# Optimization experiments

Measured on AMD Instinct MI355X. Metric: run time of the kernel, lower is better.

## Reference

```python
import jax, jax.numpy as jnp
import numpy as np

BATCH, IN_F, OUT_F = 8192, 4096, 4096


def setup_inputs() -> dict:
    key = jax.random.key(0)
    kx, kw = jax.random.split(key)
    x = jax.random.normal(kx, (BATCH, IN_F), dtype=jnp.float32)
    # weights binarized to {-1, +1} as in __init__ (uniform(-1,1) then sign)
    W = jnp.where(jax.random.normal(kw, (OUT_F, IN_F)) > 0, 1.0, -1.0).astype(jnp.float32)
    return {"x": x, "W": W}


def reference(x, W):
    # forward: input thresholded to {0,1} (x>0 -> 1, else 0), then x_bin @ W^T, no bias
    x_bin = (x > 0).astype(x.dtype)
    return jnp.matmul(x_bin, W.T)  # [batch, out_features]
```

## Files before the change

### kernel.cpp

```cpp
#include <hip/hip_runtime.h>
#include <stdint.h>

typedef __attribute__((ext_vector_type(4)))  int   v4i;
typedef __attribute__((ext_vector_type(8)))  int   v8i;
typedef __attribute__((ext_vector_type(16))) float v16f;

#define BATCH 8192
#define KDIM  4096
#define NOUT  4096
#define KB    (KDIM / 2)
#define BK_B  128
#define NT    (KDIM / 256)

__global__ __launch_bounds__(256) void pack_x4(const float* __restrict__ x,
                                               uint32_t* __restrict__ xb) {
    int t = blockIdx.x * 256 + threadIdx.x;
    const float4* p = (const float4*)x + (size_t)t * 2;
    float4 f0 = p[0];
    float4 f1 = p[1];
    uint32_t b = (f0.x > 0.f ? 0x2u        : 0u)
               | (f0.y > 0.f ? 0x20u       : 0u)
               | (f0.z > 0.f ? 0x200u      : 0u)
               | (f0.w > 0.f ? 0x2000u     : 0u)
               | (f1.x > 0.f ? 0x20000u    : 0u)
               | (f1.y > 0.f ? 0x200000u   : 0u)
               | (f1.z > 0.f ? 0x2000000u  : 0u)
               | (f1.w > 0.f ? 0x20000000u : 0u);
    xb[t] = b;
}

__global__ __launch_bounds__(256) void pack_w4(const float* __restrict__ w,
                                               uint32_t* __restrict__ wb) {
    int t = blockIdx.x * 256 + threadIdx.x;
    const float4* p = (const float4*)w + (size_t)t * 2;
    float4 f0 = p[0];
    float4 f1 = p[1];
    uint32_t b = (f0.x > 0.f ? 0x2u        : 0xAu)
               | (f0.y > 0.f ? 0x20u       : 0xA0u)
               | (f0.z > 0.f ? 0x200u      : 0xA00u)
               | (f0.w > 0.f ? 0x2000u     : 0xA000u)
               | (f1.x > 0.f ? 0x20000u    : 0xA0000u)
               | (f1.y > 0.f ? 0x200000u   : 0xA00000u)
               | (f1.z > 0.f ? 0x2000000u  : 0xA000000u)
               | (f1.w > 0.f ? 0x20000000u : 0xA0000000u);
    wb[t] = b;
}

__global__ __launch_bounds__(256, 2) void bin_gemm4(const uint8_t* __restrict__ A,
                                                    const uint8_t* __restrict__ B,
                                                    float* __restrict__ C) {
    __shared__ __align__(16) uint8_t sm[49152];

    const int tid  = threadIdx.x;
    const int w    = tid >> 6;
    const int lane = tid & 63;
    const int l31  = lane & 31;
    const int kc   = lane >> 5;
    const int rsw  = lane & 7;

    const int Mbase = blockIdx.y * 256;
    const int Nbase = blockIdx.x * 128;
    const int wm = (w >> 1) * 128;
    const int wn = (w & 1) * 64;

    const int grow = lane >> 3;
    const int swz  = ((lane & 7) ^ ((lane >> 3) & 7)) * 16;

    const uint8_t* pA = A + (size_t)(Mbase + w * 64 + grow) * KB + swz;
    const uint8_t* pB = B + (size_t)(Nbase + w * 32 + grow) * KB + swz;
    uint8_t* sA = sm;
    uint8_t* sB = sm + 32768;

    v16f acc[4][2] = {};

    for (int t = 0; t < NT; ++t) {
        const int kof = t * BK_B;

        #pragma unroll
        for (int L = 0; L < 8; ++L)
            __builtin_amdgcn_global_load_lds(
                (__attribute__((address_space(1))) void*)(pA + (size_t)(L * 8) * KB + kof),
                (__attribute__((address_space(3))) void*)(sA + (w * 64 + L * 8) * 128),
                16, 0, 0);
        #pragma unroll
        for (int L = 0; L < 4; ++L)
            __builtin_amdgcn_global_load_lds(
                (__attribute__((address_space(1))) void*)(pB + (size_t)(L * 8) * KB + kof),
                (__attribute__((address_space(3))) void*)(sB + (w * 32 + L * 8) * 128),
                16, 0, 0);
        __syncthreads();

        #pragma unroll
        for (int ks = 0; ks < 4; ++ks) {
            const int slot = ((ks * 2 + kc) ^ rsw) * 16;
            v4i bf[2];
            #pragma unroll
            for (int nb = 0; nb < 2; ++nb)
                bf[nb] = *(const v4i*)(sB + (wn + nb * 32 + l31) * 128 + slot);
            #pragma unroll
            for (int mb = 0; mb < 4; ++mb) {
                v4i af = *(const v4i*)(sA + (wm + mb * 32 + l31) * 128 + slot);
                v8i a8 = {af[0], af[1], af[2], af[3], 0, 0, 0, 0};
                #pragma unroll
                for (int nb = 0; nb < 2; ++nb) {
                    v8i b8 = {bf[nb][0], bf[nb][1], bf[nb][2], bf[nb][3], 0, 0, 0, 0};
                    acc[mb][nb] = __builtin_amdgcn_mfma_scale_f32_32x32x64_f8f6f4(
                        a8, b8, acc[mb][nb], 4, 4,
                        0, 0x7F7F7F7F, 0, 0x7F7F7F7F);
                }
            }
        }
        __syncthreads();
    }

    float* Cp = C + (size_t)(Mbase + wm + 4 * kc) * NOUT + (Nbase + wn + l31);
    #pragma unroll
    for (int mb = 0; mb < 4; ++mb)
        #pragma unroll
        for (int nb = 0; nb < 2; ++nb)
            #pragma unroll
            for (int r = 0; r < 16; ++r)
                Cp[(size_t)(mb * 32 + (r & 3) + 8 * (r >> 2)) * NOUT + nb * 32]
                    = acc[mb][nb][r];
}

extern "C" void kernel_launch(void* const* d_in, const int* in_sizes, int n_in,
                              void* d_out, int out_size, void* d_ws, size_t ws_size,
                              hipStream_t stream) {
    const float* x = (const float*)d_in[0];
    const float* W = (const float*)d_in[1];
    float* out = (float*)d_out;

    uint8_t* xb = (uint8_t*)d_ws;
    uint8_t* wb = (uint8_t*)d_ws + (size_t)BATCH * KDIM / 2;

    pack_x4<<<(BATCH * (size_t)KDIM / 8) / 256, 256, 0, stream>>>(x, (uint32_t*)xb);
    pack_w4<<<((size_t)NOUT * KDIM / 8) / 256, 256, 0, stream>>>(W, (uint32_t*)wb);

    dim3 grid(NOUT / 128, BATCH / 256);
    bin_gemm4<<<grid, 256, 0, stream>>>(xb, wb, out);
}
```

Measured before the change: 330.2 us.

## Pre-swizzle W into MFMA fragment layout, load B directly to registers, double-buffer A

The weight packing kernel now writes W in a fragment-major layout, so each lane can load its MFMA B operands straight from global memory into registers with one 16-byte read, with no LDS staging. The GEMM block grows to 512 threads over a 256x256 tile, and A tiles are double-buffered in LDS, with the next tile's async global-to-LDS load issued before computing on the current one. This aims to cut LDS traffic and sync stalls and to hide A load latency. In exchange it adds register pressure from the 8 per-iteration B fragment loads and relies on L2 for B reuse across blocks that share an N column.

```diff
diff --git a/kernel.cpp b/kernel.cpp
--- a/kernel.cpp
+++ b/kernel.cpp
@@ -29,27 +29,35 @@
     xb[t] = b;
 }
 
-__global__ __launch_bounds__(256) void pack_w4(const float* __restrict__ w,
-                                               uint32_t* __restrict__ wb) {
-    int t = blockIdx.x * 256 + threadIdx.x;
-    const float4* p = (const float4*)w + (size_t)t * 2;
-    float4 f0 = p[0];
-    float4 f1 = p[1];
-    uint32_t b = (f0.x > 0.f ? 0x2u        : 0xAu)
-               | (f0.y > 0.f ? 0x20u       : 0xA0u)
-               | (f0.z > 0.f ? 0x200u      : 0xA00u)
-               | (f0.w > 0.f ? 0x2000u     : 0xA000u)
-               | (f1.x > 0.f ? 0x20000u    : 0xA0000u)
-               | (f1.y > 0.f ? 0x200000u   : 0xA00000u)
-               | (f1.z > 0.f ? 0x2000000u  : 0xA000000u)
-               | (f1.w > 0.f ? 0x20000000u : 0xA0000000u);
-    wb[t] = b;
+__global__ __launch_bounds__(256) void pack_wf(const float* __restrict__ w,
+                                               uint32_t* __restrict__ wf) {
+    int u = blockIdx.x * 256 + threadIdx.x;
+    int lane = u & 63;
+    int T    = (u >> 6) & 63;
+    int g    = u >> 12;
+    const float* src = w + (size_t)(g * 32 + (lane & 31)) * KDIM
+                         + T * 64 + (lane >> 5) * 32;
+    uint32_t wd[4];
+    #pragma unroll
+    for (int i = 0; i < 4; ++i) {
+        float4 f0 = ((const float4*)src)[i * 2];
+        float4 f1 = ((const float4*)src)[i * 2 + 1];
+        wd[i] = (f0.x > 0.f ? 0x2u        : 0xAu)
+              | (f0.y > 0.f ? 0x20u       : 0xA0u)
+              | (f0.z > 0.f ? 0x200u      : 0xA00u)
+              | (f0.w > 0.f ? 0x2000u     : 0xA000u)
+              | (f1.x > 0.f ? 0x20000u    : 0xA0000u)
+              | (f1.y > 0.f ? 0x200000u   : 0xA00000u)
+              | (f1.z > 0.f ? 0x2000000u  : 0xA000000u)
+              | (f1.w > 0.f ? 0x20000000u : 0xA0000000u);
+    }
+    ((uint4*)wf)[u] = make_uint4(wd[0], wd[1], wd[2], wd[3]);
 }
 
-__global__ __launch_bounds__(256, 2) void bin_gemm4(const uint8_t* __restrict__ A,
-                                                    const uint8_t* __restrict__ B,
+__global__ __launch_bounds__(512, 2) void bin_gemm4(const uint8_t* __restrict__ A,
+                                                    const uint8_t* __restrict__ Bf,
                                                     float* __restrict__ C) {
-    __shared__ __align__(16) uint8_t sm[49152];
+    __shared__ __align__(16) uint8_t sm[65536];
 
     const int tid  = threadIdx.x;
     const int w    = tid >> 6;
@@ -59,57 +67,66 @@
     const int rsw  = lane & 7;
 
     const int Mbase = blockIdx.y * 256;
-    const int Nbase = blockIdx.x * 128;
-    const int wm = (w >> 1) * 128;
-    const int wn = (w & 1) * 64;
+    const int Nbase = blockIdx.x * 256;
+    const int wm = (w >> 2) * 128;
+    const int wn = (w & 3) * 64;
 
-    const int grow = lane >> 3;
+    const int srow = w * 32 + (lane >> 3);
     const int swz  = ((lane & 7) ^ ((lane >> 3) & 7)) * 16;
+    const uint8_t* pA = A + (size_t)(Mbase + srow) * KB + swz;
 
-    const uint8_t* pA = A + (size_t)(Mbase + w * 64 + grow) * KB + swz;
-    const uint8_t* pB = B + (size_t)(Nbase + w * 32 + grow) * KB + swz;
-    uint8_t* sA = sm;
-    uint8_t* sB = sm + 32768;
+    const uint8_t* pBf = Bf + (size_t)((Nbase + wn) >> 5) * 65536 + (size_t)lane * 16;
 
     v16f acc[4][2] = {};
 
+    #pragma unroll
+    for (int L = 0; L < 4; ++L)
+        __builtin_amdgcn_global_load_lds(
+            (__attribute__((address_space(1))) void*)(pA + (size_t)(L * 8) * KB),
+            (__attribute__((address_space(3))) void*)(sm + (w * 32 + L * 8) * 128),
+            16, 0, 0);
+    __syncthreads();
+
     for (int t = 0; t < NT; ++t) {
-        const int kof = t * BK_B;
+        v4i bfr[2][4];
+        #pragma unroll
+        for (int nb = 0; nb < 2; ++nb)
+            #pragma unroll
+            for (int ks = 0; ks < 4; ++ks)
+                bfr[nb][ks] = *(const v4i*)(pBf + (size_t)(nb * 64 + t * 4 + ks) * 1024);
 
-        #pragma unroll
-        for (int L = 0; L < 8; ++L)
-            __builtin_amdgcn_global_load_lds(
-                (__attribute__((address_space(1))) void*)(pA + (size_t)(L * 8) * KB + kof),
-                (__attribute__((address_space(3))) void*)(sA + (w * 64 + L * 8) * 128),
-                16, 0, 0);
-        #pragma unroll
-        for (int L = 0; L < 4; ++L)
-            __builtin_amdgcn_global_load_lds(
-                (__attribute__((address_space(1))) void*)(pB + (size_t)(L * 8) * KB + kof),
-                (__attribute__((address_space(3))) void*)(sB + (w * 32 + L * 8) * 128),
-                16, 0, 0);
-        __syncthreads();
+        if (t + 1 < NT) {
+            const int nbuf = (t + 1) & 1;
+            const int kof  = (t + 1) * BK_B;
+            #pragma unroll
+            for (int L = 0; L < 4; ++L)
+                __builtin_amdgcn_global_load_lds(
+                    (__attribute__((address_space(1))) void*)(pA + (size_t)(L * 8) * KB + kof),
+                    (__attribute__((address_space(3))) void*)(sm + nbuf * 32768 + (w * 32 + L * 8) * 128),
+                    16, 0, 0);
+        }
 
+        const uint8_t* sA = sm + (t & 1) * 32768;
         #pragma unroll
         for (int ks = 0; ks < 4; ++ks) {
             const int slot = ((ks * 2 + kc) ^ rsw) * 16;
-            v4i bf[2];
+            v8i b8[2];
             #pragma unroll
             for (int nb = 0; nb < 2; ++nb)
-                bf[nb] = *(const v4i*)(sB + (wn + nb * 32 + l31) * 128 + slot);
+                b8[nb] = (v8i){bfr[nb][ks][0], bfr[nb][ks][1],
+                               bfr[nb][ks][2], bfr[nb][ks][3], 0, 0, 0, 0};
             #pragma unroll
             for (int mb = 0; mb < 4; ++mb) {
                 v4i af = *(const v4i*)(sA + (wm + mb * 32 + l31) * 128 + slot);
                 v8i a8 = {af[0], af[1], af[2], af[3], 0, 0, 0, 0};
                 #pragma unroll
-                for (int nb = 0; nb < 2; ++nb) {
-                    v8i b8 = {bf[nb][0], bf[nb][1], bf[nb][2], bf[nb][3], 0, 0, 0, 0};
+                for (int nb = 0; nb < 2; ++nb)
                     acc[mb][nb] = __builtin_amdgcn_mfma_scale_f32_32x32x64_f8f6f4(
-                        a8, b8, acc[mb][nb], 4, 4,
+                        a8, b8[nb], acc[mb][nb], 4, 4,
                         0, 0x7F7F7F7F, 0, 0x7F7F7F7F);
-                }
             }
         }
+
         __syncthreads();
     }
 
@@ -132,11 +149,11 @@
     float* out = (float*)d_out;
 
     uint8_t* xb = (uint8_t*)d_ws;
-    uint8_t* wb = (uint8_t*)d_ws + (size_t)BATCH * KDIM / 2;
+    uint8_t* wf = (uint8_t*)d_ws + (size_t)BATCH * KDIM / 2;
 
     pack_x4<<<(BATCH * (size_t)KDIM / 8) / 256, 256, 0, stream>>>(x, (uint32_t*)xb);
-    pack_w4<<<((size_t)NOUT * KDIM / 8) / 256, 256, 0, stream>>>(W, (uint32_t*)wb);
+    pack_wf<<<(128 * 64 * 64) / 256, 256, 0, stream>>>(W, (uint32_t*)wf);
 
-    dim3 grid(NOUT / 128, BATCH / 256);
-    bin_gemm4<<<grid, 256, 0, stream>>>(xb, wb, out);
+    dim3 grid(NOUT / 256, BATCH / 256);
+    bin_gemm4<<<grid, 512, 0, stream>>>(xb, wf, out);
 }
```

Result: no change. 333.3 us (+0.9%).
